# Kernel optimization log

Hardware: AMD Instinct MI355X
Metric: run time of the kernel (lower is better)

The kernel has to match this reference:

```python
import jax, jax.numpy as jnp
import numpy as np

N_LAYERS = 6
C = 768          # hidden_channels
FC = 3072        # filter_channels
H = 12           # n_heads
KC = C // H      # k_channels = 64
KS = 3           # ffn kernel_size
W = 4            # window_size
B = 8
T = 512
EPS = 1e-5


def setup_inputs() -> dict:
    key = jax.random.key(0)
    ks = iter(jax.random.split(key, 24))
    def rn(shape, s=0.02):
        return jax.random.normal(next(ks), shape, dtype=jnp.float32) * s
    inp = {}
    inp['x'] = jax.random.normal(next(ks), (B, C, T), dtype=jnp.float32)
    inp['x_lengths'] = jax.random.randint(next(ks), (B,), T // 2, T + 1, dtype=jnp.int32)
    inp['conv_q_w'] = rn((N_LAYERS, C, C))
    inp['conv_q_b'] = rn((N_LAYERS, C))
    inp['conv_k_w'] = rn((N_LAYERS, C, C))
    inp['conv_k_b'] = rn((N_LAYERS, C))
    inp['conv_v_w'] = rn((N_LAYERS, C, C))
    inp['conv_v_b'] = rn((N_LAYERS, C))
    inp['conv_o_w'] = rn((N_LAYERS, C, C))
    inp['conv_o_b'] = rn((N_LAYERS, C))
    inp['emb_rel_k'] = rn((N_LAYERS, 1, 2 * W + 1, KC), KC ** -0.5)
    inp['emb_rel_v'] = rn((N_LAYERS, 1, 2 * W + 1, KC), KC ** -0.5)
    inp['norm1_g'] = jnp.ones((N_LAYERS, C), jnp.float32)
    inp['norm1_b'] = jnp.zeros((N_LAYERS, C), jnp.float32)
    inp['ffn_w1'] = rn((N_LAYERS, FC, C, KS))
    inp['ffn_b1'] = rn((N_LAYERS, FC))
    inp['ffn_w2'] = rn((N_LAYERS, C, FC, KS))
    inp['ffn_b2'] = rn((N_LAYERS, C))
    inp['norm2_g'] = jnp.ones((N_LAYERS, C), jnp.float32)
    inp['norm2_b'] = jnp.zeros((N_LAYERS, C), jnp.float32)
    return inp


def _layer_norm(x, g, b):
    # x: [B, C, T]; normalize over channel dim (torch code transposes then layer_norms)
    m = jnp.mean(x, axis=1, keepdims=True)
    v = jnp.mean(jnp.square(x - m), axis=1, keepdims=True)
    return (x - m) * jax.lax.rsqrt(v + EPS) * g[None, :, None] + b[None, :, None]


def _conv1d_same(x, w, b):
    # x: [B, Cin, T], w: [Cout, Cin, K], same padding ((K-1)//2, K//2)
    k = w.shape[-1]
    y = jax.lax.conv_general_dilated(x, w, (1,), [((k - 1) // 2, k // 2)],
                                     dimension_numbers=('NCH', 'OIH', 'NCH'))
    return y + b[None, :, None]


def _get_relative_embeddings(emb, length):
    # emb: [1, 2W+1, KC] -> [1, 2*length-1, KC]
    pad_l = max(length - (W + 1), 0)
    start = max(W + 1 - length, 0)
    e = jnp.pad(emb, ((0, 0), (pad_l, pad_l), (0, 0)))
    return e[:, start:start + 2 * length - 1]


def _rel_to_abs(x):
    # x: [B, H, L, 2L-1] -> [B, H, L, L]
    b, h, L, _ = x.shape
    x = jnp.pad(x, ((0, 0), (0, 0), (0, 0), (0, 1)))
    x = x.reshape(b, h, L * 2 * L)
    x = jnp.pad(x, ((0, 0), (0, 0), (0, L - 1)))
    return x.reshape(b, h, L + 1, 2 * L - 1)[:, :, :L, L - 1:]


def _abs_to_rel(x):
    # x: [B, H, L, L] -> [B, H, L, 2L-1]
    b, h, L, _ = x.shape
    x = jnp.pad(x, ((0, 0), (0, 0), (0, 0), (0, L - 1)))
    x = x.reshape(b, h, L * (2 * L - 1))
    x = jnp.pad(x, ((0, 0), (0, 0), (L, 0)))
    return x.reshape(b, h, L, 2 * L)[:, :, :, 1:]


def _encoder(x, x_lengths, conv_q_w, conv_q_b, conv_k_w, conv_k_b, conv_v_w, conv_v_b,
             conv_o_w, conv_o_b, emb_rel_k, emb_rel_v, norm1_g, norm1_b,
             ffn_w1, ffn_b1, ffn_w2, ffn_b2, norm2_g, norm2_b):
    Bn, Cc, Tt = x.shape
    mask = (jnp.arange(Tt)[None, :] < x_lengths[:, None]).astype(x.dtype)[:, None, :]  # [B,1,T]
    attn_mask = mask[:, :, :, None] * mask[:, :, None, :]  # [B,1,T,T]
    x = x * mask
    scale = KC ** -0.5
    for i in range(N_LAYERS):
        xm = x * mask
        q = jnp.einsum('bct,oc->bot', xm, conv_q_w[i]) + conv_q_b[i][None, :, None]
        k = jnp.einsum('bct,oc->bot', xm, conv_k_w[i]) + conv_k_b[i][None, :, None]
        v = jnp.einsum('bct,oc->bot', xm, conv_v_w[i]) + conv_v_b[i][None, :, None]
        # [B, C, T] -> [B, H, T, KC]
        qh = q.reshape(Bn, H, KC, Tt).transpose(0, 1, 3, 2) * scale
        kh = k.reshape(Bn, H, KC, Tt).transpose(0, 1, 3, 2)
        vh = v.reshape(Bn, H, KC, Tt).transpose(0, 1, 3, 2)
        scores = jnp.einsum('bhtd,bhsd->bhts', qh, kh)
        rel_k = _get_relative_embeddings(emb_rel_k[i], Tt)  # [1, 2T-1, KC]
        rel_logits = jnp.einsum('bhtd,rd->bhtr', qh, rel_k[0])
        scores = scores + _rel_to_abs(rel_logits)
        scores = jnp.where(attn_mask == 0, -1e4, scores)
        p = jax.nn.softmax(scores, axis=-1)
        out = jnp.einsum('bhts,bhsd->bhtd', p, vh)
        rel_w = _abs_to_rel(p)  # [B, H, T, 2T-1]
        rel_v = _get_relative_embeddings(emb_rel_v[i], Tt)
        out = out + jnp.einsum('bhtr,rd->bhtd', rel_w, rel_v[0])
        out = out.transpose(0, 1, 3, 2).reshape(Bn, Cc, Tt)
        y = jnp.einsum('bct,oc->bot', out, conv_o_w[i]) + conv_o_b[i][None, :, None]
        x = _layer_norm(x + y, norm1_g[i], norm1_b[i])
        # FFN (relu, non-causal same padding)
        h = jax.nn.relu(_conv1d_same(x * mask, ffn_w1[i], ffn_b1[i]))
        y = _conv1d_same(h * mask, ffn_w2[i], ffn_b2[i]) * mask
        x = _layer_norm(x + y, norm2_g[i], norm2_b[i])
    return x * mask


def reference(x, x_lengths, conv_q_w, conv_q_b, conv_k_w, conv_k_b, conv_v_w, conv_v_b,
              conv_o_w, conv_o_b, emb_rel_k, emb_rel_v, norm1_g, norm1_b,
              ffn_w1, ffn_b1, ffn_w2, ffn_b2, norm2_g, norm2_b):
    return _encoder(x, x_lengths, conv_q_w, conv_q_b, conv_k_w, conv_k_b, conv_v_w, conv_v_b,
                    conv_o_w, conv_o_b, emb_rel_k, emb_rel_v, norm1_g, norm1_b,
                    ffn_w1, ffn_b1, ffn_w2, ffn_b2, norm2_g, norm2_b)
```

## Files before the change

### kernel.cpp

```cpp
#include <hip/hip_runtime.h>

#define DI __device__ __forceinline__

typedef short bf16x8 __attribute__((ext_vector_type(8)));
typedef float f32x4 __attribute__((ext_vector_type(4)));
typedef unsigned short u16;

static DI float bfu2f(unsigned short u) {
    return __uint_as_float(((unsigned)u) << 16);
}
static DI unsigned short f2bu(float f) {
    unsigned u = __float_as_uint(f);
    u += 0x7fffu + ((u >> 16) & 1u);
    return (unsigned short)(u >> 16);
}

static DI void swz_block(int& bx, int& by) {
    const int gx = gridDim.x;
    const int n = gx * gridDim.y;
    const int ord = blockIdx.y * gx + blockIdx.x;
    const int cpx = n >> 3;
    const int s = (ord & 7) * cpx + (ord >> 3);
    bx = s % gx;
    by = s / gx;
}

__global__ __launch_bounds__(256) void cvt_1x1(
    const float* __restrict__ q, const float* __restrict__ k,
    const float* __restrict__ v, const float* __restrict__ o,
    u16* __restrict__ out)
{
    const int sel = blockIdx.y;
    const float* src = (sel == 0) ? q : (sel == 1) ? k : (sel == 2) ? v : o;
    const int i = blockIdx.x * 256 + threadIdx.x;
    const float4 w = ((const float4*)src)[i];
    ushort4 s;
    s.x = f2bu(w.x); s.y = f2bu(w.y); s.z = f2bu(w.z); s.w = f2bu(w.w);
    ((ushort4*)(out + (size_t)sel * 589824))[i] = s;
}

__global__ __launch_bounds__(256) void cvt_k3(
    const float* __restrict__ in, u16* __restrict__ out, int M, int K)
{
    const int i = blockIdx.x * 256 + threadIdx.x;
    const int m = i / (K / 4);
    const int c4 = (i - m * (K / 4)) * 4;
    const float* ap = in + ((size_t)m * K + c4) * 3;
    const float4 w0 = *(const float4*)ap;
    const float4 w1 = *(const float4*)(ap + 4);
    const float4 w2 = *(const float4*)(ap + 8);
    ushort4 s0, s1, s2;
    s0.x = f2bu(w0.x); s0.y = f2bu(w0.w); s0.z = f2bu(w1.z); s0.w = f2bu(w2.y);
    s1.x = f2bu(w0.y); s1.y = f2bu(w1.x); s1.z = f2bu(w1.w); s1.w = f2bu(w2.z);
    s2.x = f2bu(w0.z); s2.y = f2bu(w1.y); s2.z = f2bu(w2.x); s2.w = f2bu(w2.w);
    const size_t PS = (size_t)M * K;
    const size_t off = (size_t)m * K + c4;
    *(ushort4*)(out + off) = s0;
    *(ushort4*)(out + PS + off) = s1;
    *(ushort4*)(out + 2 * PS + off) = s2;
}

template<int BM, int BN, int BK, int KS, bool MASK_IN, bool RELU, bool MASK_OUT>
static DI void gemm_dev(const u16* __restrict__ A, size_t PS,
                        const float* __restrict__ bias,
                        const u16* __restrict__ Bin,
                        u16* __restrict__ Cout,
                        const int* __restrict__ lens,
                        int K, int ldB, int ldC, int m0, int n0)
{
    constexpr int HALO = (KS == 3) ? 1 : 0;
    constexpr int BROWS = BN + 2 * HALO;
    constexpr int MI = BM / 32;
    constexpr int NI = BN / 32;
    constexpr int AIT = KS * BM * (BK / 8) / 256;
    static_assert(KS * BM * (BK / 8) == AIT * 256, "A staging must divide evenly");

    __shared__ short As[KS][BM][BK + 8];
    __shared__ short Bs[BROWS][BK + 8];

    const int tid = threadIdx.x;
    const int batch = n0 >> 9;
    const int len0 = lens[batch];
    const int lane = tid & 63;
    const int wid = tid >> 6;
    const int wm = (wid >> 1) * (BM / 2);
    const int wn = (wid & 1) * (BN / 2);
    const int fr = lane & 15;
    const int fk = (lane >> 4) * 8;

    f32x4 acc[MI][NI];
#pragma unroll
    for (int i = 0; i < MI; ++i)
#pragma unroll
        for (int j = 0; j < NI; ++j) {
            f32x4 z = {0.f, 0.f, 0.f, 0.f};
            acc[i][j] = z;
        }

    for (int c0 = 0; c0 < K; c0 += BK) {
#pragma unroll
        for (int t = 0; t < AIT; ++t) {
            const int u = t * 256 + tid;
            const int tap = u / (BM * (BK / 8));
            const int rem = u - tap * (BM * (BK / 8));
            const int row = rem / (BK / 8);
            const int ch8 = (rem % (BK / 8)) * 8;
            const uint4 w = *(const uint4*)(
                A + (size_t)tap * PS + (size_t)(m0 + row) * K + c0 + ch8);
            *(uint4*)&As[tap][row][ch8] = w;
        }
        constexpr int BCH = BROWS * (BK / 16);
        for (int u = tid; u < BCH; u += 256) {
            const int rl = u / (BK / 16);
            const int half = (u % (BK / 16)) * 16;
            const int g = n0 + rl - HALO;
            bool valid = ((unsigned)g < 4096u) && ((g >> 9) == batch);
            if (MASK_IN && valid) valid = (g & 511) < len0;
            uint4 q0 = {0u, 0u, 0u, 0u}, q1 = {0u, 0u, 0u, 0u};
            if (valid) {
                const u16* bp = Bin + (size_t)g * ldB + c0 + half;
                q0 = *(const uint4*)bp;
                q1 = *(const uint4*)(bp + 8);
            }
            *(uint4*)&Bs[rl][half] = q0;
            *(uint4*)&Bs[rl][half + 8] = q1;
        }
        __syncthreads();
#pragma unroll
        for (int kk = 0; kk < BK; kk += 32) {
#pragma unroll
            for (int tap = 0; tap < KS; ++tap) {
                bf16x8 af[MI], bg[NI];
#pragma unroll
                for (int mi = 0; mi < MI; ++mi)
                    af[mi] = *(const bf16x8*)&As[tap][wm + mi * 16 + fr][kk + fk];
#pragma unroll
                for (int ni = 0; ni < NI; ++ni)
                    bg[ni] = *(const bf16x8*)&Bs[wn + ni * 16 + fr + tap][kk + fk];
#pragma unroll
                for (int mi = 0; mi < MI; ++mi)
#pragma unroll
                    for (int ni = 0; ni < NI; ++ni)
                        acc[mi][ni] = __builtin_amdgcn_mfma_f32_16x16x32_bf16(
                            af[mi], bg[ni], acc[mi][ni], 0, 0, 0);
            }
        }
        __syncthreads();
    }
#pragma unroll
    for (int mi = 0; mi < MI; ++mi) {
        const int m = m0 + wm + mi * 16 + (lane >> 4) * 4;
        const float4 bi = *(const float4*)(bias + m);
#pragma unroll
        for (int ni = 0; ni < NI; ++ni) {
            const int g = n0 + wn + ni * 16 + fr;
            float r0 = acc[mi][ni][0] + bi.x;
            float r1 = acc[mi][ni][1] + bi.y;
            float r2 = acc[mi][ni][2] + bi.z;
            float r3 = acc[mi][ni][3] + bi.w;
            if (RELU) {
                r0 = fmaxf(r0, 0.f); r1 = fmaxf(r1, 0.f);
                r2 = fmaxf(r2, 0.f); r3 = fmaxf(r3, 0.f);
            }
            ushort4 s;
            s.x = f2bu(r0); s.y = f2bu(r1); s.z = f2bu(r2); s.w = f2bu(r3);
            if (MASK_OUT && ((g & 511) >= len0)) { s.x = 0; s.y = 0; s.z = 0; s.w = 0; }
            *(ushort4*)(Cout + (size_t)g * ldC + m) = s;
        }
    }
}

template<int BM, int BN, int BK, int KS, bool MASK_IN, bool RELU, bool MASK_OUT>
__global__ __launch_bounds__(256) void mfma_gemm(
    const u16* __restrict__ A, size_t PS, const float* __restrict__ bias,
    const u16* __restrict__ Bin, u16* __restrict__ Cout,
    const int* __restrict__ lens, int K, int ldB, int ldC)
{
    int bx, by;
    swz_block(bx, by);
    gemm_dev<BM, BN, BK, KS, MASK_IN, RELU, MASK_OUT>(
        A, PS, bias, Bin, Cout, lens, K, ldB, ldC, by * BM, bx * BN);
}

__global__ __launch_bounds__(256) void mfma_qkv(
    const u16* __restrict__ W,
    const float* __restrict__ qb, const float* __restrict__ kb,
    const float* __restrict__ vb,
    const u16* __restrict__ Xb, u16* __restrict__ QKV,
    const int* __restrict__ lens)
{
    int bx, by;
    swz_block(bx, by);
    const int sel = by / 6;
    const int m0 = (by % 6) * 128;
    const u16* A = W + (size_t)sel * 589824;
    const float* bi = (sel == 0) ? qb : (sel == 1) ? kb : vb;
    gemm_dev<128, 128, 32, 1, true, false, false>(
        A, 0, bi, Xb, QKV + sel * 768, lens, 768, 768, 2304, m0, bx * 128);
}

__global__ __launch_bounds__(256) void transp_v(
    const u16* __restrict__ QKV, u16* __restrict__ Vt)
{
    __shared__ u16 tile[64][65];
    const int tid = threadIdx.x;
    const int bh = blockIdx.y;
    const int b = bh / 12, h = bh - b * 12;
    const int t0 = blockIdx.x * 64;
    const u16* src = QKV + ((size_t)(b * 512 + t0)) * 2304 + 1536 + h * 64;
    const int rr = tid >> 2, c0 = (tid & 3) * 16;
#pragma unroll
    for (int j = 0; j < 4; ++j) {
        const ushort4 v = *(const ushort4*)(src + (size_t)rr * 2304 + c0 + j * 4);
        tile[rr][c0 + j * 4 + 0] = v.x;
        tile[rr][c0 + j * 4 + 1] = v.y;
        tile[rr][c0 + j * 4 + 2] = v.z;
        tile[rr][c0 + j * 4 + 3] = v.w;
    }
    __syncthreads();
    const int d = tid >> 2, tc = (tid & 3) * 16;
    u16* dst = Vt + (size_t)bh * 64 * 512 + (size_t)d * 512 + t0 + tc;
#pragma unroll
    for (int j = 0; j < 4; ++j) {
        ushort4 o;
        o.x = tile[tc + j * 4 + 0][d];
        o.y = tile[tc + j * 4 + 1][d];
        o.z = tile[tc + j * 4 + 2][d];
        o.w = tile[tc + j * 4 + 3][d];
        *(ushort4*)(dst + j * 4) = o;
    }
}

__global__ __launch_bounds__(256, 4) void attn_mfma(
    const u16* __restrict__ QKV, const u16* __restrict__ Vt,
    const float* __restrict__ relk, const float* __restrict__ relv,
    const int* __restrict__ lens, u16* __restrict__ Out)
{
    const int T = 512, H = 12;
    const int tid = threadIdx.x;
    const int t0 = blockIdx.x * 16;
    const int bh = blockIdx.y;
    const int b = bh / H, h = bh - b * H;
    const int len = lens[b];

    __shared__ u16 Qs[16][72];
    __shared__ float S[16][528];
    __shared__ float RB[16][12];
    __shared__ float Lsum[16];

    const int lane = tid & 63;
    const int w = tid >> 6;
    const int fr = lane & 15;
    const int fg = lane >> 4;

    {
        const int qr = tid >> 4, d4 = (tid & 15) * 4;
        const ushort4 q4 = *(const ushort4*)(
            QKV + ((size_t)(b * 512 + t0 + qr)) * 2304 + h * 64 + d4);
        *(ushort4*)&Qs[qr][d4] = q4;
    }
    __syncthreads();

    if (tid < 144) {
        const int rr = tid / 9, o = tid - (tid / 9) * 9;
        float s = 0.f;
        for (int d = 0; d < 64; ++d) s += bfu2f(Qs[rr][d]) * relk[o * 64 + d];
        RB[rr][o] = s;
    }
    __syncthreads();

    {
        bf16x8 qa0 = *(const bf16x8*)&Qs[fr][fg * 8];
        bf16x8 qa1 = *(const bf16x8*)&Qs[fr][32 + fg * 8];
        const u16* Kbase = QKV + ((size_t)(b * 512)) * 2304 + 768 + h * 64;
        f32x4 sa[8];
#pragma unroll
        for (int f = 0; f < 8; ++f) {
            const int s0 = w * 128 + f * 16;
            const u16* kp = Kbase + (size_t)(s0 + fr) * 2304 + fg * 8;
            const bf16x8 kb0 = *(const bf16x8*)kp;
            const bf16x8 kb1 = *(const bf16x8*)(kp + 32);
            f32x4 z = {0.f, 0.f, 0.f, 0.f};
            z = __builtin_amdgcn_mfma_f32_16x16x32_bf16(qa0, kb0, z, 0, 0, 0);
            sa[f] = __builtin_amdgcn_mfma_f32_16x16x32_bf16(qa1, kb1, z, 0, 0, 0);
        }
#pragma unroll
        for (int f = 0; f < 8; ++f) {
            const int s_abs = w * 128 + f * 16 + fr;
#pragma unroll
            for (int i = 0; i < 4; ++i) {
                const int r = fg * 4 + i;
                const int t_abs = t0 + r;
                float v = sa[f][i];
                const int off = s_abs - t_abs;
                if (off >= -4 && off <= 4) v += RB[r][off + 4];
                v *= 0.125f;
                if (s_abs >= len || t_abs >= len) v = -1e4f;
                S[r][s_abs] = v;
            }
        }
    }
    __syncthreads();

    {
        const int r = tid >> 4, lx = tid & 15;
        float sv[32];
        float mx = -3.0e38f;
#pragma unroll
        for (int j = 0; j < 32; ++j) {
            sv[j] = S[r][lx + 16 * j];
            mx = fmaxf(mx, sv[j]);
        }
#pragma unroll
        for (int m = 8; m >= 1; m >>= 1) mx = fmaxf(mx, __shfl_xor(mx, m));
        char* rowp = (char*)&S[0][0] + r * 2112;
        float sum = 0.f;
#pragma unroll
        for (int j = 0; j < 32; ++j) {
            const int c = lx + 16 * j;
            const float p = __expf(sv[j] - mx);
            sum += p;
            const u16 hi = f2bu(p);
            const u16 lo = f2bu(p - bfu2f(hi));
            *(u16*)(rowp + c * 2) = hi;
            *(u16*)(rowp + 1056 + c * 2) = lo;
        }
#pragma unroll
        for (int m = 8; m >= 1; m >>= 1) sum += __shfl_xor(sum, m);
        if (lx == 0) Lsum[r] = sum;
    }
    __syncthreads();

    f32x4 oacc = {0.f, 0.f, 0.f, 0.f};
    {
        const u16* vtp = Vt + (size_t)bh * 64 * 512 + (size_t)(w * 16 + fr) * 512;
        const char* prow = (const char*)&S[0][0] + fr * 2112;
#pragma unroll 4
        for (int ks = 0; ks < 16; ++ks) {
            const int k0 = ks * 32;
            const bf16x8 pa_hi = *(const bf16x8*)(prow + (k0 + fg * 8) * 2);
            const bf16x8 pa_lo = *(const bf16x8*)(prow + 1056 + (k0 + fg * 8) * 2);
            const bf16x8 vb = *(const bf16x8*)(vtp + k0 + fg * 8);
            oacc = __builtin_amdgcn_mfma_f32_16x16x32_bf16(pa_hi, vb, oacc, 0, 0, 0);
            oacc = __builtin_amdgcn_mfma_f32_16x16x32_bf16(pa_lo, vb, oacc, 0, 0, 0);
        }
    }

    {
        const int d = w * 16 + fr;
        float rvv[9];
#pragma unroll
        for (int o = 0; o < 9; ++o) rvv[o] = relv[o * 64 + d];
        const char* Sbase = (const char*)&S[0][0];
#pragma unroll
        for (int i = 0; i < 4; ++i) {
            const int r = fg * 4 + i;
            const int t_abs = t0 + r;
            float o = oacc[i];
            const char* rp = Sbase + r * 2112;
#pragma unroll
            for (int dd = 0; dd < 9; ++dd) {
                const int s = t_abs + dd - 4;
                if (s >= 0 && s < T) {
                    const float p = bfu2f(*(const u16*)(rp + s * 2))
                                  + bfu2f(*(const u16*)(rp + 1056 + s * 2));
                    o += p * rvv[dd];
                }
            }
            o *= 1.0f / Lsum[r];
            Out[((size_t)(b * 512 + t_abs)) * 768 + h * 64 + d] = f2bu(o);
        }
    }
}

__global__ __launch_bounds__(256) void ln_kernel(
    float* __restrict__ X, const u16* __restrict__ Y,
    const float* __restrict__ g, const float* __restrict__ bb,
    u16* __restrict__ Xb)
{
    const int row = blockIdx.x * 4 + (threadIdx.x >> 6);
    const int lane = threadIdx.x & 63;
    float* xp = X + (size_t)row * 768;
    const u16* yp = Y + (size_t)row * 768;
    u16* xbp = Xb + (size_t)row * 768;
    float v[12];
    float s1 = 0.f, s2 = 0.f;
#pragma unroll
    for (int j = 0; j < 3; ++j) {
        const int c = lane * 4 + j * 256;
        const float4 x4 = *(const float4*)(xp + c);
        const ushort4 y4 = *(const ushort4*)(yp + c);
        const float a0 = x4.x + bfu2f(y4.x);
        const float a1 = x4.y + bfu2f(y4.y);
        const float a2 = x4.z + bfu2f(y4.z);
        const float a3 = x4.w + bfu2f(y4.w);
        v[j * 4 + 0] = a0; v[j * 4 + 1] = a1; v[j * 4 + 2] = a2; v[j * 4 + 3] = a3;
        s1 += a0 + a1 + a2 + a3;
        s2 += a0 * a0 + a1 * a1 + a2 * a2 + a3 * a3;
    }
#pragma unroll
    for (int m = 32; m >= 1; m >>= 1) {
        s1 += __shfl_xor(s1, m);
        s2 += __shfl_xor(s2, m);
    }
    const float mean = s1 * (1.0f / 768.0f);
    const float rstd = rsqrtf(s2 * (1.0f / 768.0f) - mean * mean + 1e-5f);
#pragma unroll
    for (int j = 0; j < 3; ++j) {
        const int c = lane * 4 + j * 256;
        const float4 g4 = *(const float4*)(g + c);
        const float4 b4 = *(const float4*)(bb + c);
        float4 o;
        o.x = (v[j * 4 + 0] - mean) * rstd * g4.x + b4.x;
        o.y = (v[j * 4 + 1] - mean) * rstd * g4.y + b4.y;
        o.z = (v[j * 4 + 2] - mean) * rstd * g4.z + b4.z;
        o.w = (v[j * 4 + 3] - mean) * rstd * g4.w + b4.w;
        *(float4*)(xp + c) = o;
        ushort4 s;
        s.x = f2bu(o.x); s.y = f2bu(o.y); s.z = f2bu(o.z); s.w = f2bu(o.w);
        *(ushort4*)(xbp + c) = s;
    }
}

__global__ __launch_bounds__(256) void transpose_in(
    const float* __restrict__ in, float* __restrict__ X, u16* __restrict__ Xb)
{
    __shared__ float tile[32][33];
    const int b = blockIdx.z;
    const int t0 = blockIdx.x * 32, c0 = blockIdx.y * 32;
    const int lx = threadIdx.x & 31, ly = threadIdx.x >> 5;
    const float* ip = in + ((size_t)b * 768 + c0) * 512 + t0;
#pragma unroll
    for (int j = 0; j < 4; ++j)
        tile[ly + j * 8][lx] = ip[(size_t)(ly + j * 8) * 512 + lx];
    __syncthreads();
    float* xp = X + ((size_t)b * 512 + t0) * 768 + c0;
    u16* xbp = Xb + ((size_t)b * 512 + t0) * 768 + c0;
#pragma unroll
    for (int j = 0; j < 4; ++j) {
        const float val = tile[lx][ly + j * 8];
        xp[(size_t)(ly + j * 8) * 768 + lx] = val;
        xbp[(size_t)(ly + j * 8) * 768 + lx] = f2bu(val);
    }
}

__global__ __launch_bounds__(256) void finalize_kernel(
    const float* __restrict__ X, const int* __restrict__ lens,
    float* __restrict__ out)
{
    __shared__ float tile[32][33];
    const int b = blockIdx.z;
    const int t0 = blockIdx.x * 32, c0 = blockIdx.y * 32;
    const int lx = threadIdx.x & 31, ly = threadIdx.x >> 5;
    const float* xp = X + ((size_t)b * 512 + t0) * 768 + c0;
#pragma unroll
    for (int j = 0; j < 4; ++j)
        tile[ly + j * 8][lx] = xp[(size_t)(ly + j * 8) * 768 + lx];
    __syncthreads();
    const int len = lens[b];
    float* op = out + ((size_t)b * 768 + c0) * 512 + t0;
    const bool on = (t0 + lx) < len;
#pragma unroll
    for (int j = 0; j < 4; ++j)
        op[(size_t)(ly + j * 8) * 512 + lx] = on ? tile[lx][ly + j * 8] : 0.0f;
}

extern "C" void kernel_launch(void* const* d_in, const int* in_sizes, int n_in,
                              void* d_out, int out_size, void* d_ws, size_t ws_size,
                              hipStream_t stream)
{
    (void)in_sizes; (void)n_in; (void)out_size; (void)ws_size;
    const int C = 768, FC = 3072, NL = 6;
    const size_t NROW = (size_t)8 * 512;

    const float* xin  = (const float*)d_in[0];
    const int*   lens = (const int*)d_in[1];
    const float* qw = (const float*)d_in[2];
    const float* qb = (const float*)d_in[3];
    const float* kw = (const float*)d_in[4];
    const float* kb = (const float*)d_in[5];
    const float* vw = (const float*)d_in[6];
    const float* vb = (const float*)d_in[7];
    const float* ow = (const float*)d_in[8];
    const float* ob = (const float*)d_in[9];
    const float* rk = (const float*)d_in[10];
    const float* rv = (const float*)d_in[11];
    const float* n1g = (const float*)d_in[12];
    const float* n1b = (const float*)d_in[13];
    const float* w1 = (const float*)d_in[14];
    const float* b1 = (const float*)d_in[15];
    const float* w2 = (const float*)d_in[16];
    const float* b2 = (const float*)d_in[17];
    const float* n2g = (const float*)d_in[18];
    const float* n2b = (const float*)d_in[19];

    char* p0 = (char*)d_ws;
    float* X = (float*)p0;
    u16* QKV = (u16*)(p0 + NROW * 768 * 4);
    u16* ATb = QKV + NROW * 2304;
    u16* Yb  = ATb + NROW * 768;
    u16* Xb  = Yb + NROW * 768;
    u16* Wc  = Xb + NROW * 768;
    u16* Hb  = QKV;
    u16* Vt  = Yb;

    transpose_in<<<dim3(16, 24, 8), 256, 0, stream>>>(xin, X, Xb);

    for (int i = 0; i < NL; ++i) {
        cvt_1x1<<<dim3(576, 4), 256, 0, stream>>>(
            qw + (size_t)i * C * C, kw + (size_t)i * C * C,
            vw + (size_t)i * C * C, ow + (size_t)i * C * C, Wc);
        mfma_qkv<<<dim3(32, 18), 256, 0, stream>>>(
            Wc, qb + i * C, kb + i * C, vb + i * C, Xb, QKV, lens);
        transp_v<<<dim3(8, 96), 256, 0, stream>>>(QKV, Vt);
        attn_mfma<<<dim3(32, 96), 256, 0, stream>>>(
            QKV, Vt, rk + (size_t)i * 9 * 64, rv + (size_t)i * 9 * 64, lens, ATb);
        mfma_gemm<64, 64, 64, 1, false, false, false><<<dim3(64, 12), 256, 0, stream>>>(
            Wc + (size_t)3 * 589824, 0, ob + i * C, ATb, Yb, lens, 768, 768, 768);
        ln_kernel<<<dim3(1024), 256, 0, stream>>>(X, Yb, n1g + i * C, n1b + i * C, Xb);
        cvt_k3<<<dim3(2304), 256, 0, stream>>>(
            w1 + (size_t)i * FC * C * 3, Wc, FC, C);
        mfma_gemm<128, 128, 32, 3, true, true, true><<<dim3(32, 24), 256, 0, stream>>>(
            Wc, (size_t)FC * C, b1 + i * FC, Xb, Hb, lens, 768, 768, 3072);
        cvt_k3<<<dim3(2304), 256, 0, stream>>>(
            w2 + (size_t)i * C * FC * 3, Wc, C, FC);
        mfma_gemm<64, 64, 64, 3, false, false, true><<<dim3(64, 12), 256, 0, stream>>>(
            Wc, (size_t)C * FC, b2 + i * C, Hb, Yb, lens, 3072, 3072, 768);
        ln_kernel<<<dim3(1024), 256, 0, stream>>>(X, Yb, n2g + i * C, n2b + i * C, Xb);
    }

    finalize_kernel<<<dim3(16, 24, 8), 256, 0, stream>>>(X, lens, (float*)d_out);
}
```

Before: 2.361 ms.

## Stage GEMM tiles via direct global-to-LDS loads with XOR swizzle

Result: faster. 1.929 ms (-18.3%).

```diff
diff --git a/kernel.cpp b/kernel.cpp
--- a/kernel.cpp
+++ b/kernel.cpp
@@ -13,6 +13,12 @@
     unsigned u = __float_as_uint(f);
     u += 0x7fffu + ((u >> 16) & 1u);
     return (unsigned short)(u >> 16);
+}
+
+static DI void gld16(const u16* g, u16* l) {
+    __builtin_amdgcn_global_load_lds(
+        (const __attribute__((address_space(1))) void*)g,
+        (__attribute__((address_space(3))) void*)l, 16, 0, 0);
 }
 
 static DI void swz_block(int& bx, int& by) {
@@ -24,6 +30,8 @@
     bx = s % gx;
     by = s / gx;
 }
+
+__global__ void zinit(u16* z) { z[threadIdx.x] = 0; }
 
 __global__ __launch_bounds__(256) void cvt_1x1(
     const float* __restrict__ q, const float* __restrict__ k,
@@ -60,23 +68,24 @@
     *(ushort4*)(out + 2 * PS + off) = s2;
 }
 
-template<int BM, int BN, int BK, int KS, bool MASK_IN, bool RELU, bool MASK_OUT>
+template<int BM, int BN, int KS, bool MASK_IN, bool RELU, bool MASK_OUT>
 static DI void gemm_dev(const u16* __restrict__ A, size_t PS,
                         const float* __restrict__ bias,
                         const u16* __restrict__ Bin,
                         u16* __restrict__ Cout,
                         const int* __restrict__ lens,
+                        const u16* __restrict__ zpage,
                         int K, int ldB, int ldC, int m0, int n0)
 {
     constexpr int HALO = (KS == 3) ? 1 : 0;
-    constexpr int BROWS = BN + 2 * HALO;
     constexpr int MI = BM / 32;
     constexpr int NI = BN / 32;
-    constexpr int AIT = KS * BM * (BK / 8) / 256;
-    static_assert(KS * BM * (BK / 8) == AIT * 256, "A staging must divide evenly");
-
-    __shared__ short As[KS][BM][BK + 8];
-    __shared__ short Bs[BROWS][BK + 8];
+    constexpr int nACH = KS * BM / 8;
+    constexpr int nBCH = BN / 8;
+    static_assert(nACH % 4 == 0 && nBCH % 4 == 0, "chunks per wave");
+
+    __shared__ __align__(16) u16 As[KS * BM][64];
+    __shared__ __align__(16) u16 Bs[BN + 2 * HALO][64];
 
     const int tid = threadIdx.x;
     const int batch = n0 >> 9;
@@ -86,7 +95,11 @@
     const int wm = (wid >> 1) * (BM / 2);
     const int wn = (wid & 1) * (BN / 2);
     const int fr = lane & 15;
-    const int fk = (lane >> 4) * 8;
+    const int fg = lane >> 4;
+    const int l8 = lane >> 3;
+    const int lg = lane & 7;
+    const int sga = lg ^ l8;
+    const int sgb = lg ^ ((HALO + l8) & 7);
 
     f32x4 acc[MI][NI];
 #pragma unroll
@@ -97,52 +110,57 @@
             acc[i][j] = z;
         }
 
-    for (int c0 = 0; c0 < K; c0 += BK) {
-#pragma unroll
-        for (int t = 0; t < AIT; ++t) {
-            const int u = t * 256 + tid;
-            const int tap = u / (BM * (BK / 8));
-            const int rem = u - tap * (BM * (BK / 8));
-            const int row = rem / (BK / 8);
-            const int ch8 = (rem % (BK / 8)) * 8;
-            const uint4 w = *(const uint4*)(
-                A + (size_t)tap * PS + (size_t)(m0 + row) * K + c0 + ch8);
-            *(uint4*)&As[tap][row][ch8] = w;
-        }
-        constexpr int BCH = BROWS * (BK / 16);
-        for (int u = tid; u < BCH; u += 256) {
-            const int rl = u / (BK / 16);
-            const int half = (u % (BK / 16)) * 16;
-            const int g = n0 + rl - HALO;
-            bool valid = ((unsigned)g < 4096u) && ((g >> 9) == batch);
-            if (MASK_IN && valid) valid = (g & 511) < len0;
-            uint4 q0 = {0u, 0u, 0u, 0u}, q1 = {0u, 0u, 0u, 0u};
-            if (valid) {
-                const u16* bp = Bin + (size_t)g * ldB + c0 + half;
-                q0 = *(const uint4*)bp;
-                q1 = *(const uint4*)(bp + 8);
-            }
-            *(uint4*)&Bs[rl][half] = q0;
-            *(uint4*)&Bs[rl][half + 8] = q1;
+    for (int c0 = 0; c0 < K; c0 += 64) {
+#pragma unroll
+        for (int c = 0; c < nACH / 4; ++c) {
+            const int ch = c * 4 + wid;
+            const int tap = (ch * 8) / BM;
+            const int row0 = (ch * 8) & (BM - 1);
+            const u16* g = A + (size_t)tap * PS
+                             + (size_t)(m0 + row0 + l8) * K + c0 + sga * 8;
+            gld16(g, &As[ch * 8][0]);
+        }
+#pragma unroll
+        for (int c = 0; c < nBCH / 4; ++c) {
+            const int ch = c * 4 + wid;
+            const int gr = n0 + ch * 8 + l8;
+            bool v = true;
+            if (MASK_IN) v = (gr & 511) < len0;
+            const u16* g = v ? (Bin + (size_t)gr * ldB + c0 + sgb * 8)
+                             : (zpage + sgb * 8);
+            gld16(g, &Bs[HALO + ch * 8][0]);
+        }
+        if (KS == 3 && tid < 16) {
+            const int hs = tid >> 3, j = tid & 7;
+            const int rl = hs * (BN + 1);
+            const int gr = n0 - 1 + hs * (BN + 1);
+            bool v = ((unsigned)gr < 4096u) && ((gr >> 9) == batch);
+            if (MASK_IN && v) v = (gr & 511) < len0;
+            uint4 q = {0u, 0u, 0u, 0u};
+            if (v) q = *(const uint4*)(Bin + (size_t)gr * ldB + c0 + j * 8);
+            *(uint4*)&Bs[rl][(j ^ (rl & 7)) * 8] = q;
         }
         __syncthreads();
 #pragma unroll
-        for (int kk = 0; kk < BK; kk += 32) {
+        for (int kh = 0; kh < 2; ++kh) {
+            const int kg = kh * 4;
 #pragma unroll
             for (int tap = 0; tap < KS; ++tap) {
-                bf16x8 af[MI], bg[NI];
+                bf16x8 af[MI], bgv[NI];
 #pragma unroll
                 for (int mi = 0; mi < MI; ++mi)
-                    af[mi] = *(const bf16x8*)&As[tap][wm + mi * 16 + fr][kk + fk];
+                    af[mi] = *(const bf16x8*)&As[tap * BM + wm + mi * 16 + fr]
+                                               [((kg + fg) ^ (fr & 7)) * 8];
 #pragma unroll
                 for (int ni = 0; ni < NI; ++ni)
-                    bg[ni] = *(const bf16x8*)&Bs[wn + ni * 16 + fr + tap][kk + fk];
+                    bgv[ni] = *(const bf16x8*)&Bs[wn + ni * 16 + fr + tap]
+                                                [((kg + fg) ^ ((fr + tap) & 7)) * 8];
 #pragma unroll
                 for (int mi = 0; mi < MI; ++mi)
 #pragma unroll
                     for (int ni = 0; ni < NI; ++ni)
                         acc[mi][ni] = __builtin_amdgcn_mfma_f32_16x16x32_bf16(
-                            af[mi], bg[ni], acc[mi][ni], 0, 0, 0);
+                            af[mi], bgv[ni], acc[mi][ni], 0, 0, 0);
             }
         }
         __syncthreads();
@@ -170,16 +188,17 @@
     }
 }
 
-template<int BM, int BN, int BK, int KS, bool MASK_IN, bool RELU, bool MASK_OUT>
+template<int BM, int BN, int KS, bool MASK_IN, bool RELU, bool MASK_OUT>
 __global__ __launch_bounds__(256) void mfma_gemm(
     const u16* __restrict__ A, size_t PS, const float* __restrict__ bias,
     const u16* __restrict__ Bin, u16* __restrict__ Cout,
-    const int* __restrict__ lens, int K, int ldB, int ldC)
+    const int* __restrict__ lens, const u16* __restrict__ zpage,
+    int K, int ldB, int ldC)
 {
     int bx, by;
     swz_block(bx, by);
-    gemm_dev<BM, BN, BK, KS, MASK_IN, RELU, MASK_OUT>(
-        A, PS, bias, Bin, Cout, lens, K, ldB, ldC, by * BM, bx * BN);
+    gemm_dev<BM, BN, KS, MASK_IN, RELU, MASK_OUT>(
+        A, PS, bias, Bin, Cout, lens, zpage, K, ldB, ldC, by * BM, bx * BN);
 }
 
 __global__ __launch_bounds__(256) void mfma_qkv(
@@ -187,16 +206,16 @@
     const float* __restrict__ qb, const float* __restrict__ kb,
     const float* __restrict__ vb,
     const u16* __restrict__ Xb, u16* __restrict__ QKV,
-    const int* __restrict__ lens)
+    const int* __restrict__ lens, const u16* __restrict__ zpage)
 {
     int bx, by;
     swz_block(bx, by);
-    const int sel = by / 6;
-    const int m0 = (by % 6) * 128;
+    const int sel = by / 12;
+    const int m0 = (by % 12) * 64;
     const u16* A = W + (size_t)sel * 589824;
     const float* bi = (sel == 0) ? qb : (sel == 1) ? kb : vb;
-    gemm_dev<128, 128, 32, 1, true, false, false>(
-        A, 0, bi, Xb, QKV + sel * 768, lens, 768, 768, 2304, m0, bx * 128);
+    gemm_dev<64, 128, 1, true, false, false>(
+        A, 0, bi, Xb, QKV + sel * 768, lens, zpage, 768, 768, 2304, m0, bx * 128);
 }
 
 __global__ __launch_bounds__(256) void transp_v(
@@ -501,31 +520,33 @@
     u16* Yb  = ATb + NROW * 768;
     u16* Xb  = Yb + NROW * 768;
     u16* Wc  = Xb + NROW * 768;
+    u16* zp  = Wc + (size_t)3 * FC * C;
     u16* Hb  = QKV;
     u16* Vt  = Yb;
 
+    zinit<<<dim3(1), 64, 0, stream>>>(zp);
     transpose_in<<<dim3(16, 24, 8), 256, 0, stream>>>(xin, X, Xb);
 
     for (int i = 0; i < NL; ++i) {
         cvt_1x1<<<dim3(576, 4), 256, 0, stream>>>(
             qw + (size_t)i * C * C, kw + (size_t)i * C * C,
             vw + (size_t)i * C * C, ow + (size_t)i * C * C, Wc);
-        mfma_qkv<<<dim3(32, 18), 256, 0, stream>>>(
-            Wc, qb + i * C, kb + i * C, vb + i * C, Xb, QKV, lens);
+        mfma_qkv<<<dim3(32, 36), 256, 0, stream>>>(
+            Wc, qb + i * C, kb + i * C, vb + i * C, Xb, QKV, lens, zp);
         transp_v<<<dim3(8, 96), 256, 0, stream>>>(QKV, Vt);
         attn_mfma<<<dim3(32, 96), 256, 0, stream>>>(
             QKV, Vt, rk + (size_t)i * 9 * 64, rv + (size_t)i * 9 * 64, lens, ATb);
-        mfma_gemm<64, 64, 64, 1, false, false, false><<<dim3(64, 12), 256, 0, stream>>>(
-            Wc + (size_t)3 * 589824, 0, ob + i * C, ATb, Yb, lens, 768, 768, 768);
+        mfma_gemm<64, 64, 1, false, false, false><<<dim3(64, 12), 256, 0, stream>>>(
+            Wc + (size_t)3 * 589824, 0, ob + i * C, ATb, Yb, lens, zp, 768, 768, 768);
         ln_kernel<<<dim3(1024), 256, 0, stream>>>(X, Yb, n1g + i * C, n1b + i * C, Xb);
         cvt_k3<<<dim3(2304), 256, 0, stream>>>(
             w1 + (size_t)i * FC * C * 3, Wc, FC, C);
-        mfma_gemm<128, 128, 32, 3, true, true, true><<<dim3(32, 24), 256, 0, stream>>>(
-            Wc, (size_t)FC * C, b1 + i * FC, Xb, Hb, lens, 768, 768, 3072);
+        mfma_gemm<64, 128, 3, true, true, true><<<dim3(32, 48), 256, 0, stream>>>(
+            Wc, (size_t)FC * C, b1 + i * FC, Xb, Hb, lens, zp, 768, 768, 3072);
         cvt_k3<<<dim3(2304), 256, 0, stream>>>(
             w2 + (size_t)i * C * FC * 3, Wc, C, FC);
-        mfma_gemm<64, 64, 64, 3, false, false, true><<<dim3(64, 12), 256, 0, stream>>>(
-            Wc, (size_t)C * FC, b2 + i * C, Hb, Yb, lens, 3072, 3072, 768);
+        mfma_gemm<64, 64, 3, false, false, true><<<dim3(64, 12), 256, 0, stream>>>(
+            Wc, (size_t)C * FC, b2 + i * C, Hb, Yb, lens, zp, 3072, 3072, 768);
         ln_kernel<<<dim3(1024), 256, 0, stream>>>(X, Yb, n2g + i * C, n2b + i * C, Xb);
     }
 
```
